# Kernel tuning notes

Measured on AMD Instinct MI355X. Metric: run time of the kernel, lower is better.

## Reference

```python
import jax, jax.numpy as jnp
import numpy as np

B, T, D, H, C = 256, 512, 256, 1024, 10
VOCAB = 3

def setup_inputs() -> dict:
    key = jax.random.key(0)
    ks = jax.random.split(key, 16)
    def kaiming(k, shape):
        fan_in = shape[0]
        return jax.random.normal(k, shape, dtype=jnp.float32) * np.sqrt(2.0 / fan_in)
    inp = {
        'x': jax.random.randint(ks[0], (B, T), 0, VOCAB),
        'emb': kaiming(ks[1], (VOCAB, D)),
        'W_gx': kaiming(ks[2], (D, H)), 'W_gh': kaiming(ks[3], (H, H)), 'b_g': jnp.zeros((H,), jnp.float32),
        'W_ix': kaiming(ks[4], (D, H)), 'W_ih': kaiming(ks[5], (H, H)), 'b_i': jnp.zeros((H,), jnp.float32),
        'W_fx': kaiming(ks[6], (D, H)), 'W_fh': kaiming(ks[7], (H, H)), 'b_f': jnp.zeros((H,), jnp.float32),
        'W_ox': kaiming(ks[8], (D, H)), 'W_oh': kaiming(ks[9], (H, H)), 'b_o': jnp.zeros((H,), jnp.float32),
        'W_ph': kaiming(ks[10], (H, C)), 'b_p': jnp.zeros((C,), jnp.float32),
    }
    return inp

def _lstm_forward(x, emb, W_gx, W_gh, b_g, W_ix, W_ih, b_i, W_fx, W_fh, b_f, W_ox, W_oh, b_o, W_ph, b_p):
    xe = emb[x]  # [B, T, D]
    # precompute input projections for all steps (same math, batched GEMM)
    Wx = jnp.concatenate([W_gx, W_ix, W_fx, W_ox], axis=1)        # [D, 4H]
    Wh = jnp.concatenate([W_gh, W_ih, W_fh, W_oh], axis=1)        # [H, 4H]
    b = jnp.concatenate([b_g, b_i, b_f, b_o], axis=0)             # [4H]
    xproj = jnp.einsum('btd,dk->tbk', xe, Wx)                     # [T, B, 4H]
    Hd = W_gh.shape[0]

    def step(carry, xp_t):
        h, c = carry
        z = jnp.tanh(xp_t + h @ Wh + b)   # NOTE: original uses tanh for ALL gates
        g, i, f, o = (z[:, :Hd], z[:, Hd:2*Hd], z[:, 2*Hd:3*Hd], z[:, 3*Hd:])
        c = g * i + c * f
        h = jnp.tanh(c) * o
        return (h, c), None

    h0 = jnp.zeros((x.shape[0], Hd), xe.dtype)
    (h, _), _ = jax.lax.scan(step, (h0, h0), xproj)
    p = h @ W_ph + b_p
    return jax.nn.log_softmax(p, axis=1)

def reference(x, emb, W_gx, W_gh, b_g, W_ix, W_ih, b_i, W_fx, W_fh, b_f, W_ox, W_oh, b_o, W_ph, b_p):
    return _lstm_forward(x, emb, W_gx, W_gh, b_g, W_ix, W_ih, b_i, W_fx, W_fh, b_f, W_ox, W_oh, b_o, W_ph, b_p)
```

## Files before the change

kernel.cpp:

```cpp
#include <hip/hip_runtime.h>
#include <hip/hip_bf16.h>

#define B_ 256
#define T_ 512
#define D_ 256
#define H_ 1024
#define C_ 10
#define KSPL 448

typedef __attribute__((ext_vector_type(8))) short short8;
typedef __attribute__((ext_vector_type(4))) float floatx4;

static __device__ __forceinline__ unsigned short f2bf(float f) {
    __hip_bfloat16 b = __float2bfloat16(f);
    return *reinterpret_cast<unsigned short*>(&b);
}
static __device__ __forceinline__ float bf2f(unsigned short u) {
    unsigned int v = ((unsigned int)u) << 16;
    return __uint_as_float(v);
}
static __device__ __forceinline__ float fast_tanh(float x) {
    float e = __expf(2.f * x);
    return 1.f - __fdividef(2.f, e + 1.f);
}

__global__ void lstm_pack_wht(const float* __restrict__ Wg,
                              const float* __restrict__ Wi,
                              const float* __restrict__ Wf,
                              const float* __restrict__ Wo,
                              unsigned short* __restrict__ WT) {
    __shared__ float tile[32][33];
    int g = blockIdx.z;
    const float* W = (g == 0) ? Wg : (g == 1) ? Wi : (g == 2) ? Wf : Wo;
    int j0 = blockIdx.x * 32;
    int k0 = blockIdx.y * 32;
    int tx = threadIdx.x & 31, ty = threadIdx.x >> 5;
    #pragma unroll
    for (int s = 0; s < 32; s += 8)
        tile[ty + s][tx] = W[(size_t)(k0 + ty + s) * H_ + j0 + tx];
    __syncthreads();
    unsigned short* out = WT + ((size_t)g << 20);
    #pragma unroll
    for (int s = 0; s < 32; s += 8)
        out[(size_t)(j0 + ty + s) * 1024 + k0 + tx] = f2bf(tile[tx][ty + s]);
}

__global__ void lstm_proj3(const float* __restrict__ emb,
                           const float* __restrict__ Wgx, const float* __restrict__ Wix,
                           const float* __restrict__ Wfx, const float* __restrict__ Wox,
                           const float* __restrict__ bg, const float* __restrict__ bi,
                           const float* __restrict__ bf_, const float* __restrict__ bo,
                           float* __restrict__ proj3) {
    int col = blockIdx.x * 256 + threadIdx.x;
    int v = blockIdx.y;
    int gate = col >> 10;
    int j = col & (H_ - 1);
    const float* Wx = (gate == 0) ? Wgx : (gate == 1) ? Wix : (gate == 2) ? Wfx : Wox;
    const float* bb = (gate == 0) ? bg : (gate == 1) ? bi : (gate == 2) ? bf_ : bo;
    float acc = bb[j];
    for (int d = 0; d < D_; ++d)
        acc += emb[v * D_ + d] * Wx[(size_t)d * H_ + j];
    proj3[(size_t)v * 4096 + col] = acc;
}

__launch_bounds__(256, 1)
__global__ void lstm_persist(const unsigned short* __restrict__ WhT,
                             const float* __restrict__ proj3,
                             const int* __restrict__ x,
                             unsigned short* __restrict__ hb0,
                             unsigned short* __restrict__ hb1,
                             int* __restrict__ flg,
                             int* __restrict__ xcdctr) {
    __shared__ unsigned short Blds[64 * 1024 + 32 * KSPL];
    __shared__ float projL[3][128];
    __shared__ int s_place;

    const int tid = threadIdx.x;

    {
        unsigned int xcc_raw;
        asm volatile("s_getreg_b32 %0, hwreg(HW_REG_XCC_ID)" : "=s"(xcc_raw));
        if (tid == 0) {
            int slot = atomicAdd(&xcdctr[xcc_raw & 7], 1);
            s_place = (int)((xcc_raw & 7) << 5) | (slot & 31);
        }
    }
    __syncthreads();
    const int xcc = s_place >> 5;
    const int cw  = s_place & 31;
    const int hc0 = cw * 32;

    {
        const int q2 = tid & 63;
        const int g = q2 >> 5;
        const int hl_ = q2 & 31;
        const int j = hc0 + hl_;
        const int xq = (hl_ & 7) << 3;
        const unsigned short* src = WhT + ((size_t)g << 20) + (size_t)j * 1024;
        const int kb0 = (tid >> 6) * 256;
        #pragma unroll
        for (int it = 0; it < 32; ++it) {
            int k = kb0 + 8 * it;
            *(short8*)(Blds + (size_t)(g * 32 + hl_) * 1024 + (k ^ xq)) =
                *(const short8*)(src + k);
        }
    }
    {
        const unsigned short* src2 = WhT + ((size_t)2 << 20);
        unsigned short* G2 = Blds + 64 * 1024;
        for (int idx = tid; idx < 32 * (KSPL / 8); idx += 256) {
            int col = idx / (KSPL / 8);
            int k = (idx - col * (KSPL / 8)) * 8;
            int xq = (col & 7) << 3;
            *(short8*)(G2 + (size_t)col * KSPL + (k ^ xq)) =
                *(const short8*)(src2 + (size_t)(hc0 + col) * 1024 + k);
        }
    }
    for (int idx = tid; idx < 384; idx += 256) {
        int v = idx >> 7, q = idx & 127;
        projL[v][q] = proj3[(size_t)v * 4096 + (size_t)(q >> 5) * 1024 + hc0 + (q & 31)];
    }
    __syncthreads();

    const int w = tid >> 6;
    const int wr = w >> 1;
    const int wc = w & 1;
    const int lane = tid & 63;
    const int lr = lane & 15;
    const int kq = lane >> 4;
    const int R0 = xcc * 32 + 16 * wr;
    const int hl = 16 * wc + lr;
    const int xorq = (hl & 7) << 3;
    const size_t abase = (size_t)(R0 + lr) * H_ + 8 * kq;
    const int crow0 = R0 + 4 * kq;

    const unsigned short* BL0 = Blds + (size_t)hl * 1024;
    const unsigned short* BL1 = Blds + (size_t)(32 + hl) * 1024;
    const unsigned short* BL2 = Blds + 64 * 1024 + (size_t)hl * KSPL;
    const unsigned short* BS2 = WhT + ((size_t)2 << 20) + (size_t)(hc0 + hl) * 1024 + 8 * kq;
    const unsigned short* BS3 = WhT + ((size_t)3 << 20) + (size_t)(hc0 + hl) * 1024 + 8 * kq;

    float creg[4] = {0.f, 0.f, 0.f, 0.f};
    unsigned short* hbuf[2] = {hb0, hb1};

    for (int t = 0; t < T_; ++t) {
        const unsigned short* h_in = hbuf[t & 1];
        unsigned short* h_out = hbuf[(t + 1) & 1];

        int tok[4];
        #pragma unroll
        for (int i = 0; i < 4; ++i)
            tok[i] = x[(size_t)(crow0 + i) * T_ + t];

        if (t > 0) {
            const int* fa = flg + ((size_t)(t - 1) * 8 + xcc) * 128;
            while (true) {
                int v = 1;
                if (lane < 32)
                    v = __hip_atomic_load(fa + lane * 4, __ATOMIC_RELAXED,
                                          __HIP_MEMORY_SCOPE_AGENT);
                if (__all(v != 0)) break;
                __builtin_amdgcn_s_sleep(1);
            }
            asm volatile("" ::: "memory");
        }

        const unsigned short* aptr = h_in + abase;
        short8 afA[8], afB[8];

        #pragma unroll
        for (int j = 0; j < 8; ++j)
            asm volatile("global_load_dwordx4 %0, %1, off offset:%2 sc0"
                         : "=&v"(afA[j]) : "v"(aptr), "n"(64 * j));

        floatx4 acc[4] = {};
        #pragma unroll
        for (int c = 0; c < 4; ++c) {
            if (c < 3) {
                if ((c & 1) == 0) {
                    #pragma unroll
                    for (int j = 0; j < 8; ++j)
                        asm volatile("global_load_dwordx4 %0, %1, off offset:%2 sc0"
                                     : "=&v"(afB[j]) : "v"(aptr), "n"(64 * (8 * (c + 1) + j)));
                } else {
                    #pragma unroll
                    for (int j = 0; j < 8; ++j)
                        asm volatile("global_load_dwordx4 %0, %1, off offset:%2 sc0"
                                     : "=&v"(afA[j]) : "v"(aptr), "n"(64 * (8 * (c + 1) + j)));
                }
                __builtin_amdgcn_sched_barrier(0);
                asm volatile("s_waitcnt vmcnt(8)" ::: "memory");
                __builtin_amdgcn_sched_barrier(0);
            } else {
                __builtin_amdgcn_sched_barrier(0);
                asm volatile("s_waitcnt vmcnt(0)" ::: "memory");
                __builtin_amdgcn_sched_barrier(0);
            }
            #pragma unroll
            for (int j = 0; j < 8; ++j) {
                const int k2 = 8 * c + j;
                const short8 a = ((c & 1) == 0) ? afA[j] : afB[j];
                const int ki = (32 * k2 + 8 * kq) ^ xorq;
                short8 b0 = *(const short8*)(BL0 + ki);
                short8 b1 = *(const short8*)(BL1 + ki);
                short8 b2, b3;
                if (k2 < 14) b2 = *(const short8*)(BL2 + ki);
                else         b2 = *(const short8*)(BS2 + 32 * k2);
                b3 = *(const short8*)(BS3 + 32 * k2);
                acc[0] = __builtin_amdgcn_mfma_f32_16x16x32_bf16(a, b0, acc[0], 0, 0, 0);
                acc[1] = __builtin_amdgcn_mfma_f32_16x16x32_bf16(a, b1, acc[1], 0, 0, 0);
                acc[2] = __builtin_amdgcn_mfma_f32_16x16x32_bf16(a, b2, acc[2], 0, 0, 0);
                acc[3] = __builtin_amdgcn_mfma_f32_16x16x32_bf16(a, b3, acc[3], 0, 0, 0);
            }
        }

        #pragma unroll
        for (int i = 0; i < 4; ++i) {
            const float* pl = projL[tok[i]];
            float zg = fast_tanh(acc[0][i] + pl[hl]);
            float zi = fast_tanh(acc[1][i] + pl[32 + hl]);
            float zf = fast_tanh(acc[2][i] + pl[64 + hl]);
            float zo = fast_tanh(acc[3][i] + pl[96 + hl]);
            float cv = zg * zi + creg[i] * zf;
            creg[i] = cv;
            h_out[(size_t)(crow0 + i) * H_ + hc0 + hl] = f2bf(fast_tanh(cv) * zo);
        }

        if (t == T_ - 1) break;

        asm volatile("s_waitcnt vmcnt(0)" ::: "memory");
        __syncthreads();
        if (tid == 0)
            __hip_atomic_exchange(flg + ((size_t)t * 8 + xcc) * 128 + cw * 4, 1,
                                  __ATOMIC_RELAXED, __HIP_MEMORY_SCOPE_AGENT);
    }
}

__global__ void lstm_final(const unsigned short* __restrict__ h,
                           const float* __restrict__ Wp,
                           const float* __restrict__ bp,
                           float* __restrict__ out) {
    int row = blockIdx.x;
    int lane = threadIdx.x;
    float acc[C_];
    #pragma unroll
    for (int cc = 0; cc < C_; ++cc) acc[cc] = 0.f;
    for (int k = lane; k < H_; k += 64) {
        float hv = bf2f(h[(size_t)row * H_ + k]);
        #pragma unroll
        for (int cc = 0; cc < C_; ++cc) acc[cc] += hv * Wp[(size_t)k * C_ + cc];
    }
    #pragma unroll
    for (int cc = 0; cc < C_; ++cc)
        #pragma unroll
        for (int off = 32; off > 0; off >>= 1)
            acc[cc] += __shfl_down(acc[cc], off);
    if (lane == 0) {
        float p[C_];
        float m = -1e30f;
        #pragma unroll
        for (int cc = 0; cc < C_; ++cc) {
            p[cc] = acc[cc] + bp[cc];
            m = fmaxf(m, p[cc]);
        }
        float se = 0.f;
        #pragma unroll
        for (int cc = 0; cc < C_; ++cc) se += expf(p[cc] - m);
        float lse = m + logf(se);
        #pragma unroll
        for (int cc = 0; cc < C_; ++cc) out[(size_t)row * C_ + cc] = p[cc] - lse;
    }
}

extern "C" void kernel_launch(void* const* d_in, const int* in_sizes, int n_in,
                              void* d_out, int out_size, void* d_ws, size_t ws_size,
                              hipStream_t stream) {
    const int* x = (const int*)d_in[0];
    const float* emb = (const float*)d_in[1];
    const float* W_gx = (const float*)d_in[2];
    const float* W_gh = (const float*)d_in[3];
    const float* b_g = (const float*)d_in[4];
    const float* W_ix = (const float*)d_in[5];
    const float* W_ih = (const float*)d_in[6];
    const float* b_i = (const float*)d_in[7];
    const float* W_fx = (const float*)d_in[8];
    const float* W_fh = (const float*)d_in[9];
    const float* b_f = (const float*)d_in[10];
    const float* W_ox = (const float*)d_in[11];
    const float* W_oh = (const float*)d_in[12];
    const float* b_o = (const float*)d_in[13];
    const float* W_ph = (const float*)d_in[14];
    const float* b_p = (const float*)d_in[15];
    float* out = (float*)d_out;

    char* ws = (char*)d_ws;
    unsigned short* WhT = (unsigned short*)ws;
    size_t off = (size_t)4 * 1024 * 1024 * 2;
    float* proj3 = (float*)(ws + off); off += 3 * 4096 * 4;
    unsigned short* hbuf0 = (unsigned short*)(ws + off); off += (size_t)B_ * H_ * 2;
    unsigned short* hbuf1 = (unsigned short*)(ws + off); off += (size_t)B_ * H_ * 2;
    int* flg = (int*)(ws + off); off += (size_t)T_ * 8 * 128 * 4;
    int* xcdctr = (int*)(ws + off); off += 8 * sizeof(int);

    lstm_pack_wht<<<dim3(32, 32, 4), 256, 0, stream>>>(W_gh, W_ih, W_fh, W_oh, WhT);
    lstm_proj3<<<dim3(16, 3), 256, 0, stream>>>(emb, W_gx, W_ix, W_fx, W_ox,
                                                b_g, b_i, b_f, b_o, proj3);
    hipMemsetAsync(hbuf0, 0, (size_t)B_ * H_ * 2, stream);
    hipMemsetAsync(flg, 0, (size_t)T_ * 8 * 128 * 4, stream);
    hipMemsetAsync(xcdctr, 0, 8 * sizeof(int), stream);

    {
        const unsigned short* a0 = WhT;
        const float* a1 = proj3; const int* a2 = x;
        unsigned short* a3 = hbuf0; unsigned short* a4 = hbuf1;
        int* a5 = flg; int* a6 = xcdctr;
        void* args[] = {&a0, &a1, &a2, &a3, &a4, &a5, &a6};
        hipLaunchCooperativeKernel((const void*)lstm_persist, dim3(256), dim3(256),
                                   args, 0, stream);
    }

    lstm_final<<<B_, 64, 0, stream>>>(hbuf0, W_ph, b_p, out);
}
```

Baseline: 5.612 ms.

## Replace block barrier with per-wave flags and split MFMA accumulator chains

Each wave now publishes its own completion flag instead of the block syncing and one thread signalling. Consumer waves poll only the flag slots for the producer waves whose rows they need, using a lane-to-slot mapping. This removes the per-step __syncthreads from the recurrent loop. Separately, MFMA accumulation alternates between two accumulator sets so that consecutive MFMAs do not depend on each other. The cost is more flag traffic and extra accumulator registers.

```diff
diff --git a/kernel.cpp b/kernel.cpp
--- a/kernel.cpp
+++ b/kernel.cpp
@@ -140,6 +140,8 @@
     const unsigned short* BS2 = WhT + ((size_t)2 << 20) + (size_t)(hc0 + hl) * 1024 + 8 * kq;
     const unsigned short* BS3 = WhT + ((size_t)3 << 20) + (size_t)(hc0 + hl) * 1024 + 8 * kq;
 
+    const int pslot = (lane >> 1) * 4 + 2 * wr + (lane & 1);
+
     float creg[4] = {0.f, 0.f, 0.f, 0.f};
     unsigned short* hbuf[2] = {hb0, hb1};
 
@@ -153,11 +155,9 @@
             tok[i] = x[(size_t)(crow0 + i) * T_ + t];
 
         if (t > 0) {
-            const int* fa = flg + ((size_t)(t - 1) * 8 + xcc) * 128;
+            const int* fp = flg + ((size_t)(t - 1) * 8 + xcc) * 128 + pslot;
             while (true) {
-                int v = 1;
-                if (lane < 32)
-                    v = __hip_atomic_load(fa + lane * 4, __ATOMIC_RELAXED,
+                int v = __hip_atomic_load(fp, __ATOMIC_RELAXED,
                                           __HIP_MEMORY_SCOPE_AGENT);
                 if (__all(v != 0)) break;
                 __builtin_amdgcn_s_sleep(1);
@@ -174,6 +174,7 @@
                          : "=&v"(afA[j]) : "v"(aptr), "n"(64 * j));
 
         floatx4 acc[4] = {};
+        floatx4 acc2[4] = {};
         #pragma unroll
         for (int c = 0; c < 4; ++c) {
             if (c < 3) {
@@ -207,20 +208,27 @@
                 if (k2 < 14) b2 = *(const short8*)(BL2 + ki);
                 else         b2 = *(const short8*)(BS2 + 32 * k2);
                 b3 = *(const short8*)(BS3 + 32 * k2);
-                acc[0] = __builtin_amdgcn_mfma_f32_16x16x32_bf16(a, b0, acc[0], 0, 0, 0);
-                acc[1] = __builtin_amdgcn_mfma_f32_16x16x32_bf16(a, b1, acc[1], 0, 0, 0);
-                acc[2] = __builtin_amdgcn_mfma_f32_16x16x32_bf16(a, b2, acc[2], 0, 0, 0);
-                acc[3] = __builtin_amdgcn_mfma_f32_16x16x32_bf16(a, b3, acc[3], 0, 0, 0);
+                if ((j & 1) == 0) {
+                    acc[0] = __builtin_amdgcn_mfma_f32_16x16x32_bf16(a, b0, acc[0], 0, 0, 0);
+                    acc[1] = __builtin_amdgcn_mfma_f32_16x16x32_bf16(a, b1, acc[1], 0, 0, 0);
+                    acc[2] = __builtin_amdgcn_mfma_f32_16x16x32_bf16(a, b2, acc[2], 0, 0, 0);
+                    acc[3] = __builtin_amdgcn_mfma_f32_16x16x32_bf16(a, b3, acc[3], 0, 0, 0);
+                } else {
+                    acc2[0] = __builtin_amdgcn_mfma_f32_16x16x32_bf16(a, b0, acc2[0], 0, 0, 0);
+                    acc2[1] = __builtin_amdgcn_mfma_f32_16x16x32_bf16(a, b1, acc2[1], 0, 0, 0);
+                    acc2[2] = __builtin_amdgcn_mfma_f32_16x16x32_bf16(a, b2, acc2[2], 0, 0, 0);
+                    acc2[3] = __builtin_amdgcn_mfma_f32_16x16x32_bf16(a, b3, acc2[3], 0, 0, 0);
+                }
             }
         }
 
         #pragma unroll
         for (int i = 0; i < 4; ++i) {
-            const float* pl = projL[tok[i]];
-            float zg = fast_tanh(acc[0][i] + pl[hl]);
-            float zi = fast_tanh(acc[1][i] + pl[32 + hl]);
-            float zf = fast_tanh(acc[2][i] + pl[64 + hl]);
-            float zo = fast_tanh(acc[3][i] + pl[96 + hl]);
+            const float* plv = projL[tok[i]];
+            float zg = fast_tanh(acc[0][i] + acc2[0][i] + plv[hl]);
+            float zi = fast_tanh(acc[1][i] + acc2[1][i] + plv[32 + hl]);
+            float zf = fast_tanh(acc[2][i] + acc2[2][i] + plv[64 + hl]);
+            float zo = fast_tanh(acc[3][i] + acc2[3][i] + plv[96 + hl]);
             float cv = zg * zi + creg[i] * zf;
             creg[i] = cv;
             h_out[(size_t)(crow0 + i) * H_ + hc0 + hl] = f2bf(fast_tanh(cv) * zo);
@@ -229,9 +237,8 @@
         if (t == T_ - 1) break;
 
         asm volatile("s_waitcnt vmcnt(0)" ::: "memory");
-        __syncthreads();
-        if (tid == 0)
-            __hip_atomic_exchange(flg + ((size_t)t * 8 + xcc) * 128 + cw * 4, 1,
+        if (lane == 0)
+            __hip_atomic_exchange(flg + ((size_t)t * 8 + xcc) * 128 + cw * 4 + w, 1,
                                   __ATOMIC_RELAXED, __HIP_MEMORY_SCOPE_AGENT);
     }
 }
```

Measured after the change: 8.450 ms. +50.6%, slower.
